# Performance work log

Hardware: AMD Instinct MI355X
Metric: run time of the kernel (lower is better)

The kernel has to match this reference:

```python
import jax, jax.numpy as jnp
import numpy as np

N_SEG = 2048
SEG_LEN = 512
D = 128


def setup_inputs() -> dict:
    key = jax.random.key(0)
    k1, = jax.random.split(key, 1)
    total = N_SEG * SEG_LEN
    x = jax.random.normal(k1, (total, D), dtype=jnp.float32)
    # sizes must sum to total_tokens; use uniform segment lengths
    sizes = jnp.full((N_SEG,), SEG_LEN, dtype=jnp.int64)
    return {"x": x, "sizes": sizes, "window_size": 3}


def reference(x, sizes, window_size):
    # Segment-prefix max: for segment i (rows [start_i, start_i+sizes_i)),
    # reduce max over the first sizes_i - window_size + 1 rows.
    n = sizes.shape[0]
    total = x.shape[0]
    ends = jnp.cumsum(sizes)            # [n] exclusive end of each segment
    starts = ends - sizes               # [n] start offset of each segment
    pos = jnp.arange(total)             # [total]
    seg_id = jnp.searchsorted(ends, pos, side="right")  # [total] segment of each row
    pos_in_seg = pos - starts[seg_id]
    valid = pos_in_seg < (sizes[seg_id] - window_size + 1)
    # route invalid (tail-of-window) rows to a dummy segment that is dropped
    ids = jnp.where(valid, seg_id, n)
    out = jax.ops.segment_max(x, ids, num_segments=n + 1)  # [n+1, D]
    return out[:n]
```

## Files before the change

### kernel.cpp

```cpp
#include <hip/hip_runtime.h>
#include <math.h>


#define BLOCK 256

typedef float f32x4 __attribute__((ext_vector_type(4)));

__device__ __forceinline__ f32x4 fmax4v(f32x4 a, f32x4 b) {
    f32x4 r;
    r.x = fmaxf(a.x, b.x);
    r.y = fmaxf(a.y, b.y);
    r.z = fmaxf(a.z, b.z);
    r.w = fmaxf(a.w, b.w);
    return r;
}

__global__ __launch_bounds__(BLOCK)
void seg_prefix_max_kernel(const float* __restrict__ x,
                           const int* __restrict__ sizes,
                           const int* __restrict__ wptr,
                           float* __restrict__ out,
                           int n_seg, int D) {
    const int seg = blockIdx.x;
    if (seg >= n_seg) return;
    const int tid = threadIdx.x;
    const int w   = *wptr;

    __shared__ int red[BLOCK];
    int partial = 0;
    for (int j = tid; j < seg; j += BLOCK) partial += sizes[j];
    red[tid] = partial;
    __syncthreads();
    for (int s = BLOCK / 2; s > 0; s >>= 1) {
        if (tid < s) red[tid] += red[tid + s];
        __syncthreads();
    }
    const int start = red[0];
    const int L     = sizes[seg] - w + 1;

    const int nc4  = D >> 2;
    const int col4 = tid & 31;
    const int rg   = tid >> 5;

    f32x4 acc = { -INFINITY, -INFINITY, -INFINITY, -INFINITY };

    if (col4 < nc4) {
        const f32x4* base  = (const f32x4*)x + (size_t)start * nc4 + col4;
        const size_t step8 = (size_t)nc4 << 3;

        const int K  = (L > rg) ? ((L - rg + 7) >> 3) : 0;
        const int k0 = ((seg & 63) * K) >> 6;

        const f32x4* p = base + (size_t)(rg + (k0 << 3)) * nc4;
        #pragma unroll 4
        for (int k = k0; k < K; ++k) {
            acc = fmax4v(acc, __builtin_nontemporal_load(p));
            p += step8;
        }
        p = base + (size_t)rg * nc4;
        #pragma unroll 4
        for (int k = 0; k < k0; ++k) {
            acc = fmax4v(acc, __builtin_nontemporal_load(p));
            p += step8;
        }
    }

    __shared__ f32x4 part[8][32];
    if (col4 < nc4) part[rg][col4] = acc;
    __syncthreads();

    if (tid < nc4) {
        f32x4 a = part[0][tid];
        #pragma unroll
        for (int j = 1; j < 8; ++j) a = fmax4v(a, part[j][tid]);
        ((f32x4*)out)[(size_t)seg * nc4 + tid] = a;
    }
}

extern "C" void kernel_launch(void* const* d_in, const int* in_sizes, int n_in,
                              void* d_out, int out_size, void* d_ws, size_t ws_size,
                              hipStream_t stream) {
    const float* x     = (const float*)d_in[0];
    const int*   sizes = (const int*)d_in[1];
    const int*   wptr  = (const int*)d_in[2];
    float*       out   = (float*)d_out;

    const int n_seg = in_sizes[1];
    const int D     = out_size / n_seg;

    seg_prefix_max_kernel<<<n_seg, BLOCK, 0, stream>>>(x, sizes, wptr, out, n_seg, D);
}
```

Baseline: 639.1 us.

## Split rows into fixed chunks with atomic max merge instead of block-per-segment

Replaces the one-block-per-segment reduction with three kernels. The first computes segment starts with a scan and fills the output with an encoded minus-infinity. The second walks 64-row chunks in a grid-stride loop and merges partial maxima through order-preserving unsigned atomicMax. The third decodes the result back to floats. This aims to balance load across blocks and drop the per-block prefix sum over sizes, at the cost of two extra launches, atomics, and a binary search per chunk.

After: 691.1 us. 8.1% more time.

```diff
diff --git a/kernel.cpp b/kernel.cpp
--- a/kernel.cpp
+++ b/kernel.cpp
@@ -3,10 +3,13 @@
 
 
 #define BLOCK 256
+#define NB_MAIN 1024
+#define CHUNK_ROWS 64
+#define MAX_SEG 2560
 
 typedef float f32x4 __attribute__((ext_vector_type(4)));
 
-__device__ __forceinline__ f32x4 fmax4v(f32x4 a, f32x4 b) {
+static __device__ __forceinline__ f32x4 fmax4v(f32x4 a, f32x4 b) {
     f32x4 r;
     r.x = fmaxf(a.x, b.x);
     r.y = fmaxf(a.y, b.y);
@@ -15,66 +18,144 @@
     return r;
 }
 
+static __device__ __forceinline__ unsigned fmap(float x) {
+    unsigned b = __float_as_uint(x);
+    return (b & 0x80000000u) ? ~b : (b | 0x80000000u);
+}
+static __device__ __forceinline__ float funmap(unsigned u) {
+    return (u & 0x80000000u) ? __uint_as_float(u ^ 0x80000000u)
+                             : __uint_as_float(~u);
+}
+
 __global__ __launch_bounds__(BLOCK)
-void seg_prefix_max_kernel(const float* __restrict__ x,
-                           const int* __restrict__ sizes,
-                           const int* __restrict__ wptr,
-                           float* __restrict__ out,
-                           int n_seg, int D) {
-    const int seg = blockIdx.x;
-    if (seg >= n_seg) return;
-    const int tid = threadIdx.x;
-    const int w   = *wptr;
+void init_kernel(const int* __restrict__ sizes, int n,
+                 unsigned* __restrict__ out_u, int out_elems,
+                 int* __restrict__ starts) {
+    if ((int)blockIdx.x == (int)gridDim.x - 1) {
+        __shared__ int ssum[BLOCK];
+        const int t = threadIdx.x;
+        const int per = (n + BLOCK - 1) / BLOCK;
+        int loc[16];
+        int s = 0;
+        for (int j = 0; j < per && j < 16; ++j) {
+            int idx = t * per + j;
+            int v = (idx < n) ? sizes[idx] : 0;
+            loc[j] = s;
+            s += v;
+        }
+        ssum[t] = s;
+        __syncthreads();
+        if (t == 0) {
+            int run = 0;
+            for (int i = 0; i < BLOCK; ++i) { int tmp = ssum[i]; ssum[i] = run; run += tmp; }
+            starts[n] = run;
+        }
+        __syncthreads();
+        int off = ssum[t];
+        for (int j = 0; j < per && j < 16; ++j) {
+            int idx = t * per + j;
+            if (idx < n) starts[idx] = off + loc[j];
+        }
+    } else {
+        const int nb = (int)gridDim.x - 1;
+        for (int i = blockIdx.x * BLOCK + threadIdx.x; i < out_elems; i += nb * BLOCK)
+            out_u[i] = 0x007FFFFFu;
+    }
+}
 
-    __shared__ int red[BLOCK];
-    int partial = 0;
-    for (int j = tid; j < seg; j += BLOCK) partial += sizes[j];
-    red[tid] = partial;
-    __syncthreads();
-    for (int s = BLOCK / 2; s > 0; s >>= 1) {
-        if (tid < s) red[tid] += red[tid + s];
-        __syncthreads();
-    }
-    const int start = red[0];
-    const int L     = sizes[seg] - w + 1;
-
+__global__ __launch_bounds__(BLOCK)
+void seg_max_dense(const float* __restrict__ x,
+                   const int* __restrict__ starts_g,
+                   const int* __restrict__ wptr,
+                   unsigned* __restrict__ out_u,
+                   int n, int D) {
+    if (n > MAX_SEG) return;
+    const int tid  = threadIdx.x;
     const int nc4  = D >> 2;
     const int col4 = tid & 31;
     const int rg   = tid >> 5;
 
-    f32x4 acc = { -INFINITY, -INFINITY, -INFINITY, -INFINITY };
+    __shared__ int st[MAX_SEG + 1];
+    for (int i = tid; i <= n; i += BLOCK) st[i] = starts_g[i];
+    __syncthreads();
+    const int total = st[n];
+    const int w     = *wptr;
+    const int n_chunks = (total + CHUNK_ROWS - 1) / CHUNK_ROWS;
 
-    if (col4 < nc4) {
-        const f32x4* base  = (const f32x4*)x + (size_t)start * nc4 + col4;
-        const size_t step8 = (size_t)nc4 << 3;
+    __shared__ f32x4 part[8][32];
 
-        const int K  = (L > rg) ? ((L - rg + 7) >> 3) : 0;
-        const int k0 = ((seg & 63) * K) >> 6;
+    for (int c = blockIdx.x; c < n_chunks; c += gridDim.x) {
+        const int r0 = c * CHUNK_ROWS;
+        const int r1 = min(r0 + CHUNK_ROWS, total);
 
-        const f32x4* p = base + (size_t)(rg + (k0 << 3)) * nc4;
-        #pragma unroll 4
-        for (int k = k0; k < K; ++k) {
-            acc = fmax4v(acc, __builtin_nontemporal_load(p));
-            p += step8;
+        int lo = 0, hi = n - 1;
+        while (lo < hi) {
+            int mid = (lo + hi + 1) >> 1;
+            if (st[mid] <= r0) lo = mid; else hi = mid - 1;
         }
-        p = base + (size_t)rg * nc4;
-        #pragma unroll 4
-        for (int k = 0; k < k0; ++k) {
-            acc = fmax4v(acc, __builtin_nontemporal_load(p));
-            p += step8;
+        const int s0 = lo;
+
+        if (r1 <= st[s0 + 1]) {
+            const int Ls   = st[s0 + 1] - st[s0] - w + 1;
+            const int vend = st[s0] + (Ls > 0 ? Ls : 0);
+            const int rend = min(r1, vend);
+            int kmax = (rend - r0 - rg + 7) >> 3;
+            kmax = kmax < 0 ? 0 : (kmax > 8 ? 8 : kmax);
+
+            f32x4 acc = { -INFINITY, -INFINITY, -INFINITY, -INFINITY };
+            const f32x4* p = (const f32x4*)x + (size_t)(r0 + rg) * nc4 + col4;
+            const size_t step = (size_t)nc4 << 3;
+            if (kmax == 8) {
+                #pragma unroll
+                for (int k = 0; k < 8; ++k) {
+                    acc = fmax4v(acc, __builtin_nontemporal_load(p));
+                    p += step;
+                }
+            } else {
+                for (int k = 0; k < kmax; ++k) {
+                    acc = fmax4v(acc, __builtin_nontemporal_load(p));
+                    p += step;
+                }
+            }
+            part[rg][col4] = acc;
+            __syncthreads();
+            if (tid < 32 && rend > r0) {
+                f32x4 a = part[0][tid];
+                #pragma unroll
+                for (int j = 1; j < 8; ++j) a = fmax4v(a, part[j][tid]);
+                unsigned* dst = out_u + ((size_t)s0 * nc4 + tid) * 4;
+                atomicMax(dst + 0, fmap(a.x));
+                atomicMax(dst + 1, fmap(a.y));
+                atomicMax(dst + 2, fmap(a.z));
+                atomicMax(dst + 3, fmap(a.w));
+            }
+            __syncthreads();
+        } else {
+            int s = s0;
+            for (int k = 0; k < 8; ++k) {
+                int r = r0 + rg + (k << 3);
+                if (r >= r1) break;
+                while (r >= st[s + 1]) ++s;
+                int Ls = st[s + 1] - st[s] - w + 1;
+                if (r - st[s] < Ls) {
+                    f32x4 v = __builtin_nontemporal_load(
+                        (const f32x4*)x + (size_t)r * nc4 + col4);
+                    unsigned* dst = out_u + ((size_t)s * nc4 + col4) * 4;
+                    atomicMax(dst + 0, fmap(v.x));
+                    atomicMax(dst + 1, fmap(v.y));
+                    atomicMax(dst + 2, fmap(v.z));
+                    atomicMax(dst + 3, fmap(v.w));
+                }
+            }
         }
     }
+}
 
-    __shared__ f32x4 part[8][32];
-    if (col4 < nc4) part[rg][col4] = acc;
-    __syncthreads();
-
-    if (tid < nc4) {
-        f32x4 a = part[0][tid];
-        #pragma unroll
-        for (int j = 1; j < 8; ++j) a = fmax4v(a, part[j][tid]);
-        ((f32x4*)out)[(size_t)seg * nc4 + tid] = a;
-    }
+__global__ __launch_bounds__(BLOCK)
+void unmap_kernel(unsigned* __restrict__ u, float* __restrict__ f, int nelem) {
+    int i = blockIdx.x * BLOCK + threadIdx.x;
+    const int strd = gridDim.x * BLOCK;
+    for (; i < nelem; i += strd) f[i] = funmap(u[i]);
 }
 
 extern "C" void kernel_launch(void* const* d_in, const int* in_sizes, int n_in,
@@ -83,10 +164,15 @@
     const float* x     = (const float*)d_in[0];
     const int*   sizes = (const int*)d_in[1];
     const int*   wptr  = (const int*)d_in[2];
-    float*       out   = (float*)d_out;
 
     const int n_seg = in_sizes[1];
     const int D     = out_size / n_seg;
 
-    seg_prefix_max_kernel<<<n_seg, BLOCK, 0, stream>>>(x, sizes, wptr, out, n_seg, D);
+    unsigned* out_u  = (unsigned*)d_out;
+    float*    out_f  = (float*)d_out;
+    int*      starts = (int*)d_ws;
+
+    init_kernel<<<65, BLOCK, 0, stream>>>(sizes, n_seg, out_u, out_size, starts);
+    seg_max_dense<<<NB_MAIN, BLOCK, 0, stream>>>(x, starts, wptr, out_u, n_seg, D);
+    unmap_kernel<<<256, BLOCK, 0, stream>>>(out_u, out_f, out_size);
 }
```
